# Performance work log

Hardware: AMD Instinct MI355X
Metric: run time of the kernel (lower is better)

Reference implementation:

```python
import math
import jax, jax.numpy as jnp
import numpy as np

V_NODES = 100000
E_EDGES = 800000
D_IN = 128
D_OUT = 128
H = 4
F_H = D_OUT // H
LEAK = 0.2


def _xavier(key, shape):
    fan_in, fan_out = shape[0], shape[1]
    lim = math.sqrt(6.0 / (fan_in + fan_out))
    return jax.random.uniform(key, shape, jnp.float32, -lim, lim)


def setup_inputs() -> dict:
    key = jax.random.key(0)
    ks = jax.random.split(key, 10)
    h = jax.random.normal(ks[0], (V_NODES, D_IN), jnp.float32)
    edge_index = jax.random.randint(ks[1], (2, E_EDGES), 0, V_NODES, jnp.int64)
    # omega in {+1, -1, 0}
    edge_weight = jax.random.randint(ks[2], (E_EDGES,), -1, 2).astype(jnp.float32)
    return {
        "h": h,
        "edge_index": edge_index,
        "edge_weight": edge_weight,
        "Wq": _xavier(ks[3], (D_IN, D_OUT)), "bq": jnp.zeros((D_OUT,), jnp.float32),
        "Wk": _xavier(ks[4], (D_IN, D_OUT)), "bk": jnp.zeros((D_OUT,), jnp.float32),
        "Wv": _xavier(ks[5], (D_IN, D_OUT)), "bv": jnp.zeros((D_OUT,), jnp.float32),
        "Wo": _xavier(ks[6], (D_OUT, D_OUT)), "bo": jnp.zeros((D_OUT,), jnp.float32),
        "We": _xavier(ks[7], (1, H)), "be": jnp.zeros((H,), jnp.float32),
        "gamma": jnp.ones((D_OUT,), jnp.float32), "beta": jnp.zeros((D_OUT,), jnp.float32),
    }


def _layer_norm(x, gamma, beta, eps=1e-5):
    mu = jnp.mean(x, axis=-1, keepdims=True)
    var = jnp.var(x, axis=-1, keepdims=True)
    return (x - mu) * jax.lax.rsqrt(var + eps) * gamma + beta


def reference(h, edge_index, edge_weight, Wq, bq, Wk, bk, Wv, bv, Wo, bo, We, be, gamma, beta):
    V = h.shape[0]
    Q = (h @ Wq + bq).reshape(V, H, F_H)
    K = (h @ Wk + bk).reshape(V, H, F_H)
    Vv = (h @ Wv + bv).reshape(V, H, F_H)

    src, tgt = edge_index[0], edge_index[1]
    # edge-aware bias: Proj(omega) with LeakyReLU, [E, H]
    edge_bias = jax.nn.leaky_relu(edge_weight[:, None] * We[0] + be, LEAK)

    # per-edge multi-head scores [E, H]
    attn_raw = jnp.einsum("ehf,ehf->eh", Q[src], K[tgt]) / math.sqrt(F_H)
    attn_raw = attn_raw + edge_bias  # ent_bias = 0 (add_entity_sim=False)
    attn_exp = jnp.exp(attn_raw)

    # degree-based softmax normalization over incoming edges of each target
    deg = jax.ops.segment_sum(attn_exp, tgt, num_segments=V) + 1e-16  # [V, H]
    attn_norm = attn_exp / deg[tgt]  # [E, H]  (dropout rate = 0)

    # weighted message aggregation: alpha * omega * (W_v h_src)
    msg = Vv[src] * attn_norm[:, :, None] * edge_weight[:, None, None]  # [E, H, F_H]
    out = jax.ops.segment_sum(msg, tgt, num_segments=V).reshape(V, H * F_H)

    out = out @ Wo + bo + h  # residual
    out = _layer_norm(out, gamma, beta)
    return jax.nn.leaky_relu(out, LEAK)
```

## Files before the change

### kernel.cpp

```cpp
#include <hip/hip_runtime.h>
#include <math.h>

#define V_NODES 100000
#define E_EDGES 800000
#define HEADS 4
#define D 128
#define LEAK 0.2f
#define NB 8

typedef __attribute__((ext_vector_type(8))) short bf16x8;
typedef __attribute__((ext_vector_type(4))) float f32x4;

__device__ __forceinline__ unsigned short f2bf(float f) {
    unsigned u = __float_as_uint(f);
    u += 0x7FFFu + ((u >> 16) & 1u);
    return (unsigned short)(u >> 16);
}

__global__ __launch_bounds__(256) void prep_w(
    const float* __restrict__ Wq, const float* __restrict__ Wk,
    const float* __restrict__ Wv,
    unsigned short* __restrict__ Wt)
{
    int idx = blockIdx.x * 256 + threadIdx.x;
    int c = idx >> 7, k = idx & 127;
    int m = c >> 7, lc = c & 127;
    const float* W = (m == 0) ? Wq : (m == 1) ? Wk : Wv;
    Wt[idx] = f2bf(W[k * D + lc]);
}

__global__ __launch_bounds__(256) void qkv_mfma(
    const float* __restrict__ h, const unsigned short* __restrict__ Wt,
    const float* __restrict__ bq, const float* __restrict__ bk,
    const float* __restrict__ bv,
    float* __restrict__ Q, float* __restrict__ K, float* __restrict__ Vv)
{
    const int wave = threadIdx.x >> 6, lane = threadIdx.x & 63;
    const int row0 = blockIdx.x * 16;
    const int col0 = wave * 96;
    const int r = lane & 15, g = lane >> 4;

    bf16x8 afrag[4];
#pragma unroll
    for (int ks = 0; ks < 4; ks++) {
        const float* ap = h + (long)(row0 + r) * D + ks * 32 + g * 8;
        float4 f0 = *(const float4*)ap;
        float4 f1 = *(const float4*)(ap + 4);
        bf16x8 a;
        a[0] = (short)f2bf(f0.x); a[1] = (short)f2bf(f0.y);
        a[2] = (short)f2bf(f0.z); a[3] = (short)f2bf(f0.w);
        a[4] = (short)f2bf(f1.x); a[5] = (short)f2bf(f1.y);
        a[6] = (short)f2bf(f1.z); a[7] = (short)f2bf(f1.w);
        afrag[ks] = a;
    }

    f32x4 acc[6];
#pragma unroll
    for (int t = 0; t < 6; t++) acc[t] = (f32x4){0.f, 0.f, 0.f, 0.f};

#pragma unroll
    for (int t = 0; t < 6; t++) {
        const unsigned short* bp = Wt + (long)(col0 + t * 16 + r) * D;
#pragma unroll
        for (int ks = 0; ks < 4; ks++) {
            bf16x8 bfrag = *(const bf16x8*)(bp + ks * 32 + g * 8);
            acc[t] = __builtin_amdgcn_mfma_f32_16x16x32_bf16(afrag[ks], bfrag, acc[t], 0, 0, 0);
        }
    }

#pragma unroll
    for (int t = 0; t < 6; t++) {
        int col = col0 + t * 16 + r;
        int m = col >> 7, lc = col & 127;
        const float* bias = (m == 0) ? bq : (m == 1) ? bk : bv;
        float* O          = (m == 0) ? Q  : (m == 1) ? K  : Vv;
        float bb = bias[lc];
#pragma unroll
        for (int q = 0; q < 4; q++) {
            int R = row0 + g * 4 + q;
            O[(long)R * D + lc] = acc[t][q] + bb;
        }
    }
}

__global__ __launch_bounds__(256) void score_kernel(
    const int* __restrict__ src, const int* __restrict__ tgt,
    const float* __restrict__ ew,
    const float* __restrict__ Q, const float* __restrict__ K,
    const float* __restrict__ We, const float* __restrict__ be,
    float* __restrict__ attn_exp)
{
    int t = blockIdx.x * 256 + threadIdx.x;
    int e = t >> 4;
    int sub = t & 15;
    if (e >= E_EDGES) return;
    int s = src[e], tg = tgt[e];
    const float4* q4 = (const float4*)(Q + (long)s * D);
    const float4* k4 = (const float4*)(K + (long)tg * D);
    float4 a0 = q4[sub * 2], a1 = q4[sub * 2 + 1];
    float4 b0 = k4[sub * 2], b1 = k4[sub * 2 + 1];
    float p = a0.x * b0.x + a0.y * b0.y + a0.z * b0.z + a0.w * b0.w
            + a1.x * b1.x + a1.y * b1.y + a1.z * b1.z + a1.w * b1.w;
    p += __shfl_xor(p, 1);
    p += __shfl_xor(p, 2);
    if ((sub & 3) == 0) {
        int hh = sub >> 2;
        float w = ew[e];
        float bias = w * We[hh] + be[hh];
        bias = (bias > 0.f) ? bias : LEAK * bias;
        attn_exp[(long)e * 4 + hh] = __expf(p * 0.17677669529663687f + bias);
    }
}

__global__ __launch_bounds__(256) void hist_kernel(
    const int* __restrict__ tgt, int* __restrict__ rs)
{
    int e = blockIdx.x * 256 + threadIdx.x;
    if (e < E_EDGES) atomicAdd(&rs[tgt[e]], 1);
}

__global__ __launch_bounds__(1024) void scan_kernel(int* __restrict__ rs)
{
    __shared__ int part[1024];
    const int tid = threadIdx.x;
    const int CH = (V_NODES + 1023) / 1024;
    int begin = tid * CH;
    int end = begin + CH; if (end > V_NODES) end = V_NODES;
    if (begin > V_NODES) begin = V_NODES;
    int s = 0;
    for (int i = begin; i < end; i++) s += rs[i];
    part[tid] = s;
    __syncthreads();
    for (int off = 1; off < 1024; off <<= 1) {
        int v = (tid >= off) ? part[tid - off] : 0;
        __syncthreads();
        part[tid] += v;
        __syncthreads();
    }
    int excl = (tid == 0) ? 0 : part[tid - 1];
    for (int i = begin; i < end; i++) {
        int c = rs[i];
        rs[i] = excl;
        excl += c;
    }
}

__global__ __launch_bounds__(256) void scatter_kernel(
    const int* __restrict__ tgt, int* __restrict__ rs, int* __restrict__ csr_e)
{
    int e = blockIdx.x * 256 + threadIdx.x;
    if (e >= E_EDGES) return;
    int pos = atomicAdd(&rs[tgt[e]], 1);
    csr_e[pos] = e;
}

__global__ __launch_bounds__(256) void agg_kernel(
    const int* __restrict__ rs, const int* __restrict__ csr_e,
    const int* __restrict__ src, const float* __restrict__ ew,
    const float* __restrict__ attn_exp,
    const float* __restrict__ Vv, float* __restrict__ out)
{
    int node = blockIdx.x * 4 + (threadIdx.x >> 6);
    if (node >= V_NODES) return;
    int lane = threadIdx.x & 63;
    int hh = lane >> 4;
    int j1 = rs[node];
    int j0 = node ? rs[node - 1] : 0;
    float acc0 = 0.f, acc1 = 0.f, deg = 0.f;
    for (int j = j0; j < j1; j++) {
        int e = csr_e[j];
        float4 att = *((const float4*)(attn_exp + (long)e * 4));
        float atth = (hh == 0) ? att.x : (hh == 1) ? att.y : (hh == 2) ? att.z : att.w;
        deg += atth;
        float w = ew[e];
        if (w != 0.f) {
            float2 v = ((const float2*)(Vv + (long)src[e] * D))[lane];
            float a = atth * w;
            acc0 += a * v.x;
            acc1 += a * v.y;
        }
    }
    float inv = 1.f / (deg + 1e-16f);
    ((float2*)(out + (long)node * D))[lane] = make_float2(acc0 * inv, acc1 * inv);
}

__global__ __launch_bounds__(128) void out_kernel(
    const float* __restrict__ h, const float* __restrict__ Wo,
    const float* __restrict__ bo, const float* __restrict__ gamma,
    const float* __restrict__ beta, float* __restrict__ out)
{
    __shared__ float ash[D][NB];
    __shared__ float red[2][NB][2];
    const int tid  = threadIdx.x;
    const int base = blockIdx.x * NB;
    const int wave = tid >> 6, lane = tid & 63;

#pragma unroll
    for (int n = 0; n < NB; n++) ash[tid][n] = out[(long)(base + n) * D + tid];
    __syncthreads();

    float acc[NB];
#pragma unroll
    for (int n = 0; n < NB; n++) acc[n] = 0.f;
    for (int k = 0; k < D; k++) {
        float w = Wo[k * D + tid];
#pragma unroll
        for (int n = 0; n < NB; n++) acc[n] += ash[k][n] * w;
    }

    float bb = bo[tid];
    float v[NB];
#pragma unroll
    for (int n = 0; n < NB; n++) {
        v[n] = acc[n] + bb + h[(long)(base + n) * D + tid];
        float s = v[n], q = v[n] * v[n];
#pragma unroll
        for (int off = 32; off; off >>= 1) {
            s += __shfl_xor(s, off);
            q += __shfl_xor(q, off);
        }
        if (lane == 0) { red[wave][n][0] = s; red[wave][n][1] = q; }
    }
    __syncthreads();

    float g = gamma[tid], bt = beta[tid];
#pragma unroll
    for (int n = 0; n < NB; n++) {
        float s  = red[0][n][0] + red[1][n][0];
        float q  = red[0][n][1] + red[1][n][1];
        float mu = s * (1.f / 128.f);
        float var = q * (1.f / 128.f) - mu * mu;
        float rstd = rsqrtf(var + 1e-5f);
        float y = (v[n] - mu) * rstd * g + bt;
        out[(long)(base + n) * D + tid] = (y > 0.f) ? y : LEAK * y;
    }
}

extern "C" void kernel_launch(void* const* d_in, const int* in_sizes, int n_in,
                              void* d_out, int out_size, void* d_ws, size_t ws_size,
                              hipStream_t stream)
{
    const float* h     = (const float*)d_in[0];
    const int*   ei    = (const int*)d_in[1];
    const float* ew    = (const float*)d_in[2];
    const float* Wq    = (const float*)d_in[3];
    const float* bq    = (const float*)d_in[4];
    const float* Wk    = (const float*)d_in[5];
    const float* bk    = (const float*)d_in[6];
    const float* Wv    = (const float*)d_in[7];
    const float* bv    = (const float*)d_in[8];
    const float* Wo    = (const float*)d_in[9];
    const float* bo    = (const float*)d_in[10];
    const float* We    = (const float*)d_in[11];
    const float* be    = (const float*)d_in[12];
    const float* gamma = (const float*)d_in[13];
    const float* beta  = (const float*)d_in[14];
    float* out = (float*)d_out;

    const size_t VD = (size_t)V_NODES * D;
    float* Qf       = (float*)d_ws;
    float* Kf       = Qf + VD;
    float* Vf       = Kf + VD;
    float* attn_exp = Vf + VD;
    unsigned short* Wt = (unsigned short*)(attn_exp + (size_t)E_EDGES * 4);
    int* rs    = (int*)Qf;
    int* csr_e = rs + V_NODES;

    const int* srcp = ei;
    const int* tgtp = ei + E_EDGES;

    prep_w<<<(384 * 128) / 256, 256, 0, stream>>>(Wq, Wk, Wv, Wt);
    qkv_mfma<<<V_NODES / 16, 256, 0, stream>>>(h, Wt, bq, bk, bv, Qf, Kf, Vf);
    score_kernel<<<(E_EDGES * 16) / 256, 256, 0, stream>>>(srcp, tgtp, ew, Qf, Kf, We, be, attn_exp);

    hipMemsetAsync(rs, 0, V_NODES * sizeof(int), stream);
    hist_kernel<<<(E_EDGES + 255) / 256, 256, 0, stream>>>(tgtp, rs);
    scan_kernel<<<1, 1024, 0, stream>>>(rs);
    scatter_kernel<<<(E_EDGES + 255) / 256, 256, 0, stream>>>(tgtp, rs, csr_e);

    agg_kernel<<<(V_NODES + 3) / 4, 256, 0, stream>>>(rs, csr_e, srcp, ew, attn_exp, Vf, out);
    out_kernel<<<V_NODES / NB, 128, 0, stream>>>(h, Wo, bo, gamma, beta, out);
}
```

Measured before the change: 847.0 us.

## Pre-gather CSR-ordered packed edge data and bf16 V for aggregation

Adds a pass that gathers src, edge weight and attention exponents into CSR order, packing src with weight into one word and the four head scores into bf16 pairs. A second pass converts V to bf16. The aggregation kernel then reads these contiguous streams instead of doing indirect lookups through csr_e. This cuts the random-access bytes per edge, at the cost of two extra kernel launches, extra passes over memory, and bf16 rounding of attention and V values.

```diff
diff --git a/kernel.cpp b/kernel.cpp
--- a/kernel.cpp
+++ b/kernel.cpp
@@ -154,11 +154,38 @@
     csr_e[pos] = e;
 }
 
+__global__ __launch_bounds__(256) void csr_gather(
+    const int* __restrict__ csr_e, const int* __restrict__ src,
+    const float* __restrict__ ew, const float* __restrict__ attn_exp,
+    unsigned* __restrict__ csr_srcew, uint2* __restrict__ csr_att)
+{
+    int pos = blockIdx.x * 256 + threadIdx.x;
+    if (pos >= E_EDGES) return;
+    int e = csr_e[pos];
+    float4 a = *(const float4*)(attn_exp + (long)e * 4);
+    uint2 packed;
+    packed.x = (unsigned)f2bf(a.x) | ((unsigned)f2bf(a.y) << 16);
+    packed.y = (unsigned)f2bf(a.z) | ((unsigned)f2bf(a.w) << 16);
+    csr_att[pos] = packed;
+    int s = src[e];
+    int w = (int)ew[e] + 1;
+    csr_srcew[pos] = (unsigned)s | ((unsigned)w << 24);
+}
+
+__global__ __launch_bounds__(256) void conv_v(
+    const float* __restrict__ Vf, unsigned short* __restrict__ Vb)
+{
+    long i = ((long)blockIdx.x * 256 + threadIdx.x) * 4;
+    float4 v = *(const float4*)(Vf + i);
+    ushort4 o;
+    o.x = f2bf(v.x); o.y = f2bf(v.y); o.z = f2bf(v.z); o.w = f2bf(v.w);
+    *(ushort4*)(Vb + i) = o;
+}
+
 __global__ __launch_bounds__(256) void agg_kernel(
-    const int* __restrict__ rs, const int* __restrict__ csr_e,
-    const int* __restrict__ src, const float* __restrict__ ew,
-    const float* __restrict__ attn_exp,
-    const float* __restrict__ Vv, float* __restrict__ out)
+    const int* __restrict__ rs, const unsigned* __restrict__ csr_srcew,
+    const uint2* __restrict__ csr_att,
+    const unsigned short* __restrict__ Vb, float* __restrict__ out)
 {
     int node = blockIdx.x * 4 + (threadIdx.x >> 6);
     if (node >= V_NODES) return;
@@ -167,17 +194,19 @@
     int j1 = rs[node];
     int j0 = node ? rs[node - 1] : 0;
     float acc0 = 0.f, acc1 = 0.f, deg = 0.f;
+#pragma unroll 2
     for (int j = j0; j < j1; j++) {
-        int e = csr_e[j];
-        float4 att = *((const float4*)(attn_exp + (long)e * 4));
-        float atth = (hh == 0) ? att.x : (hh == 1) ? att.y : (hh == 2) ? att.z : att.w;
+        unsigned u = csr_srcew[j];
+        uint2 av = csr_att[j];
+        unsigned aw = (hh < 2) ? av.x : av.y;
+        float atth = __uint_as_float((hh & 1) ? (aw & 0xFFFF0000u) : (aw << 16));
         deg += atth;
-        float w = ew[e];
-        if (w != 0.f) {
-            float2 v = ((const float2*)(Vv + (long)src[e] * D))[lane];
-            float a = atth * w;
-            acc0 += a * v.x;
-            acc1 += a * v.y;
+        int w = (int)(u >> 24) - 1;
+        if (w != 0) {
+            unsigned vv = *(const unsigned*)(Vb + (long)(u & 0xFFFFFFu) * D + lane * 2);
+            float a = atth * (float)w;
+            acc0 += a * __uint_as_float(vv << 16);
+            acc1 += a * __uint_as_float(vv & 0xFFFF0000u);
         }
     }
     float inv = 1.f / (deg + 1e-16f);
@@ -263,8 +292,13 @@
     float* Vf       = Kf + VD;
     float* attn_exp = Vf + VD;
     unsigned short* Wt = (unsigned short*)(attn_exp + (size_t)E_EDGES * 4);
-    int* rs    = (int*)Qf;
-    int* csr_e = rs + V_NODES;
+
+    char* qbase = (char*)Qf;
+    int*            rs        = (int*)qbase;
+    int*            csr_e     = (int*)(qbase + 400000);
+    unsigned*       csr_srcew = (unsigned*)(qbase + 3600000);
+    uint2*          csr_att   = (uint2*)(qbase + 6800000);
+    unsigned short* Vb        = (unsigned short*)(qbase + 13200000);
 
     const int* srcp = ei;
     const int* tgtp = ei + E_EDGES;
@@ -277,7 +311,9 @@
     hist_kernel<<<(E_EDGES + 255) / 256, 256, 0, stream>>>(tgtp, rs);
     scan_kernel<<<1, 1024, 0, stream>>>(rs);
     scatter_kernel<<<(E_EDGES + 255) / 256, 256, 0, stream>>>(tgtp, rs, csr_e);
-
-    agg_kernel<<<(V_NODES + 3) / 4, 256, 0, stream>>>(rs, csr_e, srcp, ew, attn_exp, Vf, out);
+    csr_gather<<<E_EDGES / 256, 256, 0, stream>>>(csr_e, srcp, ew, attn_exp, csr_srcew, csr_att);
+    conv_v<<<(int)(VD / 4 / 256), 256, 0, stream>>>(Vf, Vb);
+
+    agg_kernel<<<(V_NODES + 3) / 4, 256, 0, stream>>>(rs, csr_srcew, csr_att, Vb, out);
     out_kernel<<<V_NODES / NB, 128, 0, stream>>>(h, Wo, bo, gamma, beta, out);
 }
```

Result: faster. 788.6 us (-6.9%).
